# Kernel optimization log

Measured on AMD Instinct MI355X. Metric: run time of the kernel, lower is better.

Reference implementation:

```python
import jax, jax.numpy as jnp
import numpy as np

B, T, E = 4, 2048, 1024
H, D = 16, 64  # n_heads, head_size


def setup_inputs() -> dict:
    key = jax.random.key(0)
    ks = jax.random.split(key, 6)
    s = 0.02
    x = jax.random.normal(ks[0], (B, T, E), dtype=jnp.float32)
    Wq = jax.random.normal(ks[1], (H, E, D), dtype=jnp.float32) * s
    Wk = jax.random.normal(ks[2], (H, E, D), dtype=jnp.float32) * s
    Wv = jax.random.normal(ks[3], (H, E, D), dtype=jnp.float32) * s
    Wp = jax.random.normal(ks[4], (E, E), dtype=jnp.float32) * s
    bp = jnp.zeros((E,), dtype=jnp.float32)
    return {"x": x, "Wq": Wq, "Wk": Wk, "Wv": Wv, "Wp": Wp, "bp": bp}


def reference(x, Wq, Wk, Wv, Wp, bp):
    # Per-head bias-free Q/K/V projections (vectorized over heads)
    q = jnp.einsum('bte,hed->bhtd', x, Wq)
    k = jnp.einsum('bte,hed->bhtd', x, Wk)
    v = jnp.einsum('bte,hed->bhtd', x, Wv)
    scale = 1.0 / jnp.sqrt(jnp.asarray(D, dtype=x.dtype))
    scores = jnp.einsum('bhtd,bhsd->bhts', q, k) * scale  # [B,H,T,T]
    causal = jnp.tril(jnp.ones((T, T), dtype=bool))
    scores = jnp.where(causal, scores, jnp.asarray(-jnp.inf, dtype=scores.dtype))
    attn = jax.nn.softmax(scores, axis=-1)
    out = jnp.einsum('bhts,bhsd->bhtd', attn, v)  # [B,H,T,D]
    # concat heads: 'nh b t c -> b t (nh c)'
    out = out.transpose(0, 2, 1, 3).reshape(B, T, H * D)
    # output projection (dropout p=0.0 is identity)
    return out @ Wp.T + bp
```

## Files before the change

### kernel.cpp

```cpp
#include <hip/hip_runtime.h>

typedef unsigned short u16;
typedef __attribute__((ext_vector_type(8))) short bf16x8;
typedef __attribute__((ext_vector_type(4))) short bf16x4;
typedef __attribute__((ext_vector_type(4))) float f32x4;

__device__ __forceinline__ u16 f2bf(float f) {
  unsigned u = __float_as_uint(f);
  u += 0x7FFFu + ((u >> 16) & 1u);
  return (u16)(u >> 16);
}
__device__ __forceinline__ unsigned pack2(float a, float b) {
  return (unsigned)f2bf(a) | ((unsigned)f2bf(b) << 16);
}
#if __has_builtin(__builtin_amdgcn_cvt_pk_bf16_f32)
typedef __attribute__((ext_vector_type(2))) __bf16 bf16v2;
__device__ __forceinline__ unsigned cvt_pk(float a, float b) {
  bf16v2 v = __builtin_amdgcn_cvt_pk_bf16_f32(a, b);
  return __builtin_bit_cast(unsigned, v);
}
#else
__device__ __forceinline__ unsigned cvt_pk(float a, float b) { return pack2(a, b); }
#endif
__device__ __forceinline__ uint4 pack8(float4 a, float4 b) {
  uint4 r;
  r.x = cvt_pk(a.x, a.y); r.y = cvt_pk(a.z, a.w);
  r.z = cvt_pk(b.x, b.y); r.w = cvt_pk(b.z, b.w);
  return r;
}
__device__ __forceinline__ void gload16(const void* g, void* l) {
  __builtin_amdgcn_global_load_lds(
      (const __attribute__((address_space(1))) void*)g,
      (__attribute__((address_space(3))) void*)l, 16, 0, 0);
}
__device__ __forceinline__ f32x4 mfma16(bf16x4 a, bf16x4 b, f32x4 c) {
#if __has_builtin(__builtin_amdgcn_mfma_f32_16x16x16bf16_1k)
  return __builtin_amdgcn_mfma_f32_16x16x16bf16_1k(a, b, c, 0, 0, 0);
#elif __has_builtin(__builtin_amdgcn_mfma_f32_16x16x16_bf16)
  return __builtin_amdgcn_mfma_f32_16x16x16_bf16(a, b, c, 0, 0, 0);
#else
  asm volatile("v_mfma_f32_16x16x16_bf16 %0, %1, %2, %0\n\ts_nop 2"
               : "+v"(c) : "v"(a), "v"(b));
  return c;
#endif
}

__global__ __launch_bounds__(256) void prep(
    const float* __restrict__ x, u16* __restrict__ xbf,
    const float* __restrict__ Wq, const float* __restrict__ Wk,
    const float* __restrict__ Wv, u16* __restrict__ wt,
    const float* __restrict__ Wp, u16* __restrict__ wpbf) {
  const int tid = threadIdx.x;
  const int b = blockIdx.x;
  __shared__ __align__(16) u16 tile[64 * 72];
  if (b < 4096) {
    const size_t i = (size_t)b * 256 + tid;
    const float4* p = (const float4*)(x + i * 8);
    *(uint4*)(xbf + i * 8) = pack8(p[0], p[1]);
  } else if (b < 4864) {
    const int idx = b - 4096;
    const int w = idx >> 8;
    const int mat = (idx >> 4) & 15;
    const int r0 = (idx & 15) * 64;
    const float* src = (w == 0 ? Wq : (w == 1 ? Wk : Wv)) + (size_t)mat * 1024 * 64;
    u16* dst = wt + (size_t)w * 1024 * 1024 + (size_t)mat * 1024 * 64;
#pragma unroll
    for (int i = 0; i < 2; ++i) {
      const int c = tid + i * 256;
      const int r = c >> 3, off = (c & 7) * 8;
      const float* p = src + (size_t)(r0 + r) * 64 + off;
      *(uint4*)(&tile[r * 72 + off]) = pack8(*(const float4*)p, *(const float4*)(p + 4));
    }
    __syncthreads();
#pragma unroll
    for (int i = 0; i < 2; ++i) {
      const int c = tid + i * 256;
      const int d = c >> 3, roff = (c & 7) * 8;
      bf16x8 v;
#pragma unroll
      for (int j = 0; j < 8; ++j) v[j] = (short)tile[(roff + j) * 72 + d];
      *(bf16x8*)(dst + (size_t)d * 1024 + r0 + roff) = v;
    }
  } else {
    const size_t i = (size_t)(b - 4864) * 256 + tid;
    const float4* p = (const float4*)(Wp + i * 8);
    *(uint4*)(wpbf + i * 8) = pack8(p[0], p[1]);
  }
}

template <int MODE>
__global__ __launch_bounds__(256) void gemm_bt(
    const u16* __restrict__ A, const u16* __restrict__ BT,
    u16* __restrict__ o0, u16* __restrict__ o1, u16* __restrict__ o2,
    float* __restrict__ fout, const float* __restrict__ bp) {
  __shared__ __align__(16) u16 As[2][128 * 32];
  __shared__ __align__(16) u16 Bs[2][128 * 32];
  const int tid = threadIdx.x;
  const int lane = tid & 63, wv = tid >> 6;
  const int g = lane >> 4, ln = lane & 15;
  const int wm = wv >> 1, wn = wv & 1;
  const int m0 = blockIdx.x * 128, n0 = blockIdx.y * 128;

  const f32x4 fz = {0.f, 0.f, 0.f, 0.f};
  f32x4 acc[4][4];
#pragma unroll
  for (int i = 0; i < 4; ++i)
#pragma unroll
    for (int j = 0; j < 4; ++j) acc[i][j] = fz;

  for (int k0 = 0; k0 < 1024; k0 += 64) {
    __syncthreads();
#pragma unroll
    for (int hf = 0; hf < 2; ++hf)
#pragma unroll
      for (int j = 0; j < 2; ++j) {
        const int c = j * 256 + tid;
        const int r = c >> 2, off = (c & 3) * 8;
        gload16(A + (size_t)(m0 + r) * 1024 + k0 + hf * 32 + off, &As[hf][c * 8]);
        gload16(BT + (size_t)(n0 + r) * 1024 + k0 + hf * 32 + off, &Bs[hf][c * 8]);
      }
    __syncthreads();
#pragma unroll
    for (int hf = 0; hf < 2; ++hf) {
      bf16x8 af[4], bfr[4];
#pragma unroll
      for (int rt = 0; rt < 4; ++rt)
        af[rt] = *(const bf16x8*)(&As[hf][(wm * 64 + rt * 16 + ln) * 32 + g * 8]);
#pragma unroll
      for (int ct = 0; ct < 4; ++ct)
        bfr[ct] = *(const bf16x8*)(&Bs[hf][(wn * 64 + ct * 16 + ln) * 32 + g * 8]);
#pragma unroll
      for (int rt = 0; rt < 4; ++rt)
#pragma unroll
        for (int ct = 0; ct < 4; ++ct)
          acc[rt][ct] = __builtin_amdgcn_mfma_f32_16x16x32_bf16(af[rt], bfr[ct],
                                                                acc[rt][ct], 0, 0, 0);
    }
  }

  if (MODE == 0) {
    const int which = n0 >> 10;
    const int nl0 = (n0 & 1023) + wn * 64;
    const float qs = (which == 0) ? 0.1803368801f : 1.0f;
    if (which < 2) {
      u16* outp = which == 0 ? o0 : o1;
#pragma unroll
      for (int rt = 0; rt < 4; ++rt)
#pragma unroll
        for (int ct = 0; ct < 4; ++ct) {
          const int nl = nl0 + ct * 16 + ln;
          const int h = nl >> 6, d = nl & 63;
          const unsigned p01 = cvt_pk(acc[rt][ct][0] * qs, acc[rt][ct][1] * qs);
          const unsigned p23 = cvt_pk(acc[rt][ct][2] * qs, acc[rt][ct][3] * qs);
          const u16 vv[4] = {(u16)p01, (u16)(p01 >> 16), (u16)p23, (u16)(p23 >> 16)};
#pragma unroll
          for (int r = 0; r < 4; ++r) {
            const int m = m0 + wm * 64 + rt * 16 + 4 * g + r;
            const int b = m >> 11, t = m & 2047;
            outp[(((size_t)(b * 16 + h) * 2048 + t) << 6) + d] = vv[r];
          }
        }
    } else {
#pragma unroll
      for (int rt = 0; rt < 4; ++rt) {
        const int tb = m0 + wm * 64 + rt * 16 + 4 * g;
        const int b = tb >> 11, t = tb & 2047;
#pragma unroll
        for (int ct = 0; ct < 4; ++ct) {
          const int nl = nl0 + ct * 16 + ln;
          const int h = nl >> 6, d = nl & 63;
          uint2 pv;
          pv.x = cvt_pk(acc[rt][ct][0], acc[rt][ct][1]);
          pv.y = cvt_pk(acc[rt][ct][2], acc[rt][ct][3]);
          *(uint2*)(o2 + ((size_t)((b * 16 + h) * 64 + d) << 11) + t) = pv;
        }
      }
    }
  } else {
#pragma unroll
    for (int ct = 0; ct < 4; ++ct) {
      const int n = n0 + wn * 64 + ct * 16 + ln;
      const float bias = bp[n];
#pragma unroll
      for (int rt = 0; rt < 4; ++rt)
#pragma unroll
        for (int r = 0; r < 4; ++r) {
          const int m = m0 + wm * 64 + rt * 16 + 4 * g + r;
          fout[(size_t)m * 1024 + n] = acc[rt][ct][r] + bias;
        }
    }
  }
}

__global__ __launch_bounds__(256) void attn_kernel(
    const u16* __restrict__ Q, const u16* __restrict__ K,
    const u16* __restrict__ VT, u16* __restrict__ AO) {
  const int tid = threadIdx.x;
  const int wv = tid >> 6, lane = tid & 63, g = lane >> 4, ln = lane & 15;
  const int bh = blockIdx.x;
  const int jb = blockIdx.y;
  const u16* Qb = Q + (size_t)bh * (2048 * 64);
  const u16* Kb = K + (size_t)bh * (2048 * 64);
  const u16* Vb = VT + (size_t)bh * (64 * 2048);

  __shared__ __align__(16) u16 Ks[64 * 72];
  __shared__ __align__(16) u16 Vs[64 * 72];

  const int sr0 = tid >> 3, so0 = (tid & 7) * 8;
  const int sr1 = sr0 + 32;

  uint4 kpf0 = *(const uint4*)(Kb + (size_t)sr0 * 64 + so0);
  uint4 kpf1 = *(const uint4*)(Kb + (size_t)sr1 * 64 + so0);
  uint4 vpf0 = *(const uint4*)(Vb + (size_t)sr0 * 2048 + so0);
  uint4 vpf1 = *(const uint4*)(Vb + (size_t)sr1 * 2048 + so0);

  const int b = bh >> 4, h = bh & 15;
  const short ob = 0x3F80;
  const bf16x4 ones = {ob, ob, ob, ob};
  const f32x4 fz = {0.f, 0.f, 0.f, 0.f};

#pragma unroll
  for (int ph = 0; ph < 2; ++ph) {
    const int qi = (ph == 0) ? jb : 15 - jb;
    const int q0 = qi * 128;
    const int nt = 2 * qi + 2;
    const int ntw = 2 * qi + 1 + (wv >> 1);

    bf16x8 qa[2][2];
#pragma unroll
    for (int rt = 0; rt < 2; ++rt) {
      const int row = q0 + wv * 32 + rt * 16 + ln;
#pragma unroll
      for (int hh = 0; hh < 2; ++hh)
        qa[rt][hh] = *(const bf16x8*)(Qb + (size_t)row * 64 + hh * 32 + g * 8);
    }

    f32x4 oacc[2][4], lacc[2];
#pragma unroll
    for (int rt = 0; rt < 2; ++rt) {
      lacc[rt] = fz;
#pragma unroll
      for (int dt = 0; dt < 4; ++dt) oacc[rt][dt] = fz;
    }

    for (int kt = 0; kt < nt; ++kt) {
      __syncthreads();
      *(uint4*)(&Ks[sr0 * 72 + so0]) = kpf0;
      *(uint4*)(&Ks[sr1 * 72 + so0]) = kpf1;
      *(uint4*)(&Vs[sr0 * 72 + so0]) = vpf0;
      *(uint4*)(&Vs[sr1 * 72 + so0]) = vpf1;
      __syncthreads();
      if ((kt + 1 < nt) || (ph == 0)) {
        const int sn = (kt + 1 < nt) ? (kt + 1) * 64 : 0;
        kpf0 = *(const uint4*)(Kb + (size_t)(sn + sr0) * 64 + so0);
        kpf1 = *(const uint4*)(Kb + (size_t)(sn + sr1) * 64 + so0);
        vpf0 = *(const uint4*)(Vb + (size_t)sr0 * 2048 + sn + so0);
        vpf1 = *(const uint4*)(Vb + (size_t)sr1 * 2048 + sn + so0);
      }
      if (kt < ntw) {
        const int s0 = kt * 64;
        f32x4 sfT[2][4];
#pragma unroll
        for (int st = 0; st < 4; ++st) {
          const bf16x8 kb0 = *(const bf16x8*)(&Ks[(st * 16 + ln) * 72 + g * 8]);
          const bf16x8 kb1 = *(const bf16x8*)(&Ks[(st * 16 + ln) * 72 + 32 + g * 8]);
#pragma unroll
          for (int rt = 0; rt < 2; ++rt) {
            sfT[rt][st] = __builtin_amdgcn_mfma_f32_16x16x32_bf16(kb0, qa[rt][0],
                                                                  fz, 0, 0, 0);
            sfT[rt][st] = __builtin_amdgcn_mfma_f32_16x16x32_bf16(kb1, qa[rt][1],
                                                                  sfT[rt][st], 0, 0, 0);
          }
        }
        const bool diag = (kt == ntw - 1);
        bf16x4 pa[2][4];
#pragma unroll
        for (int rt = 0; rt < 2; ++rt) {
          const int qloc = wv * 32 + rt * 16 + ln;
#pragma unroll
          for (int st = 0; st < 4; ++st) {
            float e[4];
#pragma unroll
            for (int r = 0; r < 4; ++r) e[r] = __builtin_amdgcn_exp2f(sfT[rt][st][r]);
            if (diag) {
              const int sloc = s0 - q0 + st * 16 + 4 * g;
#pragma unroll
              for (int r = 0; r < 4; ++r)
                if (sloc + r > qloc) e[r] = 0.f;
            }
            uint2 packed = {cvt_pk(e[0], e[1]), cvt_pk(e[2], e[3])};
            pa[rt][st] = __builtin_bit_cast(bf16x4, packed);
          }
        }
#pragma unroll
        for (int st = 0; st < 4; ++st) {
#pragma unroll
          for (int dt = 0; dt < 4; ++dt) {
            const bf16x4 vb =
                *(const bf16x4*)(&Vs[(dt * 16 + ln) * 72 + st * 16 + 4 * g]);
#pragma unroll
            for (int rt = 0; rt < 2; ++rt)
              oacc[rt][dt] = mfma16(pa[rt][st], vb, oacc[rt][dt]);
          }
#pragma unroll
          for (int rt = 0; rt < 2; ++rt)
            lacc[rt] = mfma16(pa[rt][st], ones, lacc[rt]);
        }
      }
    }
#pragma unroll
    for (int rt = 0; rt < 2; ++rt) {
      float linv[4];
#pragma unroll
      for (int r = 0; r < 4; ++r) linv[r] = 1.f / lacc[rt][r];
#pragma unroll
      for (int dt = 0; dt < 4; ++dt) {
        const unsigned p01 =
            cvt_pk(oacc[rt][dt][0] * linv[0], oacc[rt][dt][1] * linv[1]);
        const unsigned p23 =
            cvt_pk(oacc[rt][dt][2] * linv[2], oacc[rt][dt][3] * linv[3]);
        const u16 vv[4] = {(u16)p01, (u16)(p01 >> 16), (u16)p23, (u16)(p23 >> 16)};
#pragma unroll
        for (int r = 0; r < 4; ++r) {
          const int qg = q0 + wv * 32 + rt * 16 + 4 * g + r;
          AO[(size_t)(b * 2048 + qg) * 1024 + h * 64 + dt * 16 + ln] = vv[r];
        }
      }
    }
  }
}

extern "C" void kernel_launch(void* const* d_in, const int* in_sizes, int n_in,
                              void* d_out, int out_size, void* d_ws, size_t ws_size,
                              hipStream_t stream) {
  const float* x  = (const float*)d_in[0];
  const float* Wq = (const float*)d_in[1];
  const float* Wk = (const float*)d_in[2];
  const float* Wv = (const float*)d_in[3];
  const float* Wp = (const float*)d_in[4];
  const float* bp = (const float*)d_in[5];
  float* out = (float*)d_out;

  char* ws = (char*)d_ws;
  const size_t MB = 1048576;
  u16* xbf  = (u16*)(ws);
  u16* aows = (u16*)(ws);
  u16* wt   = (u16*)(ws + 16 * MB);
  u16* wpbf = (u16*)(ws + 22 * MB);
  u16* qws  = (u16*)(ws + 24 * MB);
  u16* kws  = (u16*)(ws + 40 * MB);
  u16* vtws = (u16*)(ws + 56 * MB);

  prep<<<dim3(5376), 256, 0, stream>>>(x, xbf, Wq, Wk, Wv, wt, Wp, wpbf);
  gemm_bt<0><<<dim3(64, 24), 256, 0, stream>>>(xbf, wt, qws, kws, vtws,
                                               nullptr, nullptr);
  attn_kernel<<<dim3(64, 8), 256, 0, stream>>>(qws, kws, vtws, aows);
  gemm_bt<1><<<dim3(64, 8), 256, 0, stream>>>(aows, wpbf, nullptr, nullptr,
                                              nullptr, out, bp);
}
```

Before: 263.4 us.

## Process both paired query blocks in one pass sharing K/V tile loads

The attention kernel previously ran two sequential phases, one for the light query block and one for the mirrored heavy block, reloading K/V tiles from global memory for each. It now keeps Q fragments and accumulators for both blocks live and streams K/V once over the longer range, applying QK, exp/mask and PV for each block only where it is still active. This removes the duplicate K/V global loads and LDS staging, and halves the barrier count for the shorter block. In exchange, register pressure roughly doubles for accumulators and Q fragments, which can lower occupancy or cause spills.

```diff
diff --git a/kernel.cpp b/kernel.cpp
--- a/kernel.cpp
+++ b/kernel.cpp
@@ -209,105 +209,134 @@
   const int sr0 = tid >> 3, so0 = (tid & 7) * 8;
   const int sr1 = sr0 + 32;
 
+  const int qiA = jb, qiB = 15 - jb;
+  const int q0A = qiA * 128, q0B = qiB * 128;
+  const int ntB = 2 * qiB + 2;
+  const int ntwA = 2 * qiA + 1 + (wv >> 1);
+  const int ntwB = 2 * qiB + 1 + (wv >> 1);
+
   uint4 kpf0 = *(const uint4*)(Kb + (size_t)sr0 * 64 + so0);
   uint4 kpf1 = *(const uint4*)(Kb + (size_t)sr1 * 64 + so0);
   uint4 vpf0 = *(const uint4*)(Vb + (size_t)sr0 * 2048 + so0);
   uint4 vpf1 = *(const uint4*)(Vb + (size_t)sr1 * 2048 + so0);
 
-  const int b = bh >> 4, h = bh & 15;
+  bf16x8 qaA[2][2], qaB[2][2];
+#pragma unroll
+  for (int rt = 0; rt < 2; ++rt) {
+    const int rowA = q0A + wv * 32 + rt * 16 + ln;
+    const int rowB = q0B + wv * 32 + rt * 16 + ln;
+#pragma unroll
+    for (int hh = 0; hh < 2; ++hh) {
+      qaA[rt][hh] = *(const bf16x8*)(Qb + (size_t)rowA * 64 + hh * 32 + g * 8);
+      qaB[rt][hh] = *(const bf16x8*)(Qb + (size_t)rowB * 64 + hh * 32 + g * 8);
+    }
+  }
+
+  const f32x4 fz = {0.f, 0.f, 0.f, 0.f};
+  f32x4 oaccA[2][4], oaccB[2][4], laccA[2], laccB[2];
+#pragma unroll
+  for (int rt = 0; rt < 2; ++rt) {
+    laccA[rt] = fz; laccB[rt] = fz;
+#pragma unroll
+    for (int dt = 0; dt < 4; ++dt) { oaccA[rt][dt] = fz; oaccB[rt][dt] = fz; }
+  }
+
   const short ob = 0x3F80;
   const bf16x4 ones = {ob, ob, ob, ob};
-  const f32x4 fz = {0.f, 0.f, 0.f, 0.f};
-
-#pragma unroll
-  for (int ph = 0; ph < 2; ++ph) {
-    const int qi = (ph == 0) ? jb : 15 - jb;
-    const int q0 = qi * 128;
-    const int nt = 2 * qi + 2;
-    const int ntw = 2 * qi + 1 + (wv >> 1);
-
-    bf16x8 qa[2][2];
+
+  auto expmask = [&](f32x4 (&sf)[2][4], bf16x4 (&pa)[2][4], bool diag, int s0q) {
 #pragma unroll
     for (int rt = 0; rt < 2; ++rt) {
-      const int row = q0 + wv * 32 + rt * 16 + ln;
-#pragma unroll
-      for (int hh = 0; hh < 2; ++hh)
-        qa[rt][hh] = *(const bf16x8*)(Qb + (size_t)row * 64 + hh * 32 + g * 8);
-    }
-
-    f32x4 oacc[2][4], lacc[2];
-#pragma unroll
-    for (int rt = 0; rt < 2; ++rt) {
-      lacc[rt] = fz;
-#pragma unroll
-      for (int dt = 0; dt < 4; ++dt) oacc[rt][dt] = fz;
-    }
-
-    for (int kt = 0; kt < nt; ++kt) {
-      __syncthreads();
-      *(uint4*)(&Ks[sr0 * 72 + so0]) = kpf0;
-      *(uint4*)(&Ks[sr1 * 72 + so0]) = kpf1;
-      *(uint4*)(&Vs[sr0 * 72 + so0]) = vpf0;
-      *(uint4*)(&Vs[sr1 * 72 + so0]) = vpf1;
-      __syncthreads();
-      if ((kt + 1 < nt) || (ph == 0)) {
-        const int sn = (kt + 1 < nt) ? (kt + 1) * 64 : 0;
-        kpf0 = *(const uint4*)(Kb + (size_t)(sn + sr0) * 64 + so0);
-        kpf1 = *(const uint4*)(Kb + (size_t)(sn + sr1) * 64 + so0);
-        vpf0 = *(const uint4*)(Vb + (size_t)sr0 * 2048 + sn + so0);
-        vpf1 = *(const uint4*)(Vb + (size_t)sr1 * 2048 + sn + so0);
-      }
-      if (kt < ntw) {
-        const int s0 = kt * 64;
-        f32x4 sfT[2][4];
-#pragma unroll
-        for (int st = 0; st < 4; ++st) {
-          const bf16x8 kb0 = *(const bf16x8*)(&Ks[(st * 16 + ln) * 72 + g * 8]);
-          const bf16x8 kb1 = *(const bf16x8*)(&Ks[(st * 16 + ln) * 72 + 32 + g * 8]);
-#pragma unroll
-          for (int rt = 0; rt < 2; ++rt) {
-            sfT[rt][st] = __builtin_amdgcn_mfma_f32_16x16x32_bf16(kb0, qa[rt][0],
-                                                                  fz, 0, 0, 0);
-            sfT[rt][st] = __builtin_amdgcn_mfma_f32_16x16x32_bf16(kb1, qa[rt][1],
-                                                                  sfT[rt][st], 0, 0, 0);
-          }
-        }
-        const bool diag = (kt == ntw - 1);
-        bf16x4 pa[2][4];
+      const int qloc = wv * 32 + rt * 16 + ln;
+#pragma unroll
+      for (int st = 0; st < 4; ++st) {
+        float e[4];
+#pragma unroll
+        for (int r = 0; r < 4; ++r) e[r] = __builtin_amdgcn_exp2f(sf[rt][st][r]);
+        if (diag) {
+          const int sloc = s0q + st * 16 + 4 * g;
+#pragma unroll
+          for (int r = 0; r < 4; ++r)
+            if (sloc + r > qloc) e[r] = 0.f;
+        }
+        uint2 packed = {cvt_pk(e[0], e[1]), cvt_pk(e[2], e[3])};
+        pa[rt][st] = __builtin_bit_cast(bf16x4, packed);
+      }
+    }
+  };
+
+  for (int kt = 0; kt < ntB; ++kt) {
+    __syncthreads();
+    *(uint4*)(&Ks[sr0 * 72 + so0]) = kpf0;
+    *(uint4*)(&Ks[sr1 * 72 + so0]) = kpf1;
+    *(uint4*)(&Vs[sr0 * 72 + so0]) = vpf0;
+    *(uint4*)(&Vs[sr1 * 72 + so0]) = vpf1;
+    __syncthreads();
+    if (kt + 1 < ntB) {
+      const int sn = (kt + 1) * 64;
+      kpf0 = *(const uint4*)(Kb + (size_t)(sn + sr0) * 64 + so0);
+      kpf1 = *(const uint4*)(Kb + (size_t)(sn + sr1) * 64 + so0);
+      vpf0 = *(const uint4*)(Vb + (size_t)sr0 * 2048 + sn + so0);
+      vpf1 = *(const uint4*)(Vb + (size_t)sr1 * 2048 + sn + so0);
+    }
+    const bool actA = kt < ntwA;
+    const bool actB = kt < ntwB;
+
+    f32x4 sfA[2][4], sfB[2][4];
+#pragma unroll
+    for (int st = 0; st < 4; ++st) {
+      const bf16x8 kb0 = *(const bf16x8*)(&Ks[(st * 16 + ln) * 72 + g * 8]);
+      const bf16x8 kb1 = *(const bf16x8*)(&Ks[(st * 16 + ln) * 72 + 32 + g * 8]);
+      if (actA)
 #pragma unroll
         for (int rt = 0; rt < 2; ++rt) {
-          const int qloc = wv * 32 + rt * 16 + ln;
-#pragma unroll
-          for (int st = 0; st < 4; ++st) {
-            float e[4];
-#pragma unroll
-            for (int r = 0; r < 4; ++r) e[r] = __builtin_amdgcn_exp2f(sfT[rt][st][r]);
-            if (diag) {
-              const int sloc = s0 - q0 + st * 16 + 4 * g;
-#pragma unroll
-              for (int r = 0; r < 4; ++r)
-                if (sloc + r > qloc) e[r] = 0.f;
-            }
-            uint2 packed = {cvt_pk(e[0], e[1]), cvt_pk(e[2], e[3])};
-            pa[rt][st] = __builtin_bit_cast(bf16x4, packed);
-          }
-        }
-#pragma unroll
-        for (int st = 0; st < 4; ++st) {
-#pragma unroll
-          for (int dt = 0; dt < 4; ++dt) {
-            const bf16x4 vb =
-                *(const bf16x4*)(&Vs[(dt * 16 + ln) * 72 + st * 16 + 4 * g]);
-#pragma unroll
-            for (int rt = 0; rt < 2; ++rt)
-              oacc[rt][dt] = mfma16(pa[rt][st], vb, oacc[rt][dt]);
-          }
+          sfA[rt][st] = __builtin_amdgcn_mfma_f32_16x16x32_bf16(kb0, qaA[rt][0],
+                                                                fz, 0, 0, 0);
+          sfA[rt][st] = __builtin_amdgcn_mfma_f32_16x16x32_bf16(kb1, qaA[rt][1],
+                                                                sfA[rt][st], 0, 0, 0);
+        }
+      if (actB)
+#pragma unroll
+        for (int rt = 0; rt < 2; ++rt) {
+          sfB[rt][st] = __builtin_amdgcn_mfma_f32_16x16x32_bf16(kb0, qaB[rt][0],
+                                                                fz, 0, 0, 0);
+          sfB[rt][st] = __builtin_amdgcn_mfma_f32_16x16x32_bf16(kb1, qaB[rt][1],
+                                                                sfB[rt][st], 0, 0, 0);
+        }
+    }
+    bf16x4 paA[2][4], paB[2][4];
+    const int s0 = kt * 64;
+    if (actA) expmask(sfA, paA, kt == ntwA - 1, s0 - q0A);
+    if (actB) expmask(sfB, paB, kt == ntwB - 1, s0 - q0B);
+
+#pragma unroll
+    for (int st = 0; st < 4; ++st) {
+#pragma unroll
+      for (int dt = 0; dt < 4; ++dt) {
+        const bf16x4 vb =
+            *(const bf16x4*)(&Vs[(dt * 16 + ln) * 72 + st * 16 + 4 * g]);
+        if (actA)
 #pragma unroll
           for (int rt = 0; rt < 2; ++rt)
-            lacc[rt] = mfma16(pa[rt][st], ones, lacc[rt]);
-        }
-      }
-    }
+            oaccA[rt][dt] = mfma16(paA[rt][st], vb, oaccA[rt][dt]);
+        if (actB)
+#pragma unroll
+          for (int rt = 0; rt < 2; ++rt)
+            oaccB[rt][dt] = mfma16(paB[rt][st], vb, oaccB[rt][dt]);
+      }
+      if (actA)
+#pragma unroll
+        for (int rt = 0; rt < 2; ++rt)
+          laccA[rt] = mfma16(paA[rt][st], ones, laccA[rt]);
+      if (actB)
+#pragma unroll
+        for (int rt = 0; rt < 2; ++rt)
+          laccB[rt] = mfma16(paB[rt][st], ones, laccB[rt]);
+    }
+  }
+
+  const int b = bh >> 4, h = bh & 15;
+  auto epi = [&](f32x4 (&oacc)[2][4], f32x4 (&lacc)[2], int q0) {
 #pragma unroll
     for (int rt = 0; rt < 2; ++rt) {
       float linv[4];
@@ -327,7 +356,9 @@
         }
       }
     }
-  }
+  };
+  epi(oaccA, laccA, q0A);
+  epi(oaccB, laccB, q0B);
 }
 
 extern "C" void kernel_launch(void* const* d_in, const int* in_sizes, int n_in,
```

Measured after the change: 320.9 us. +21.8%, slower.

## Load K/V fragments directly from global memory instead of staging through LDS

Applied to the files above, without the earlier changes.

The attention kernel drops the shared-memory K/V tiles, the register prefetch and both block barriers per key tile. Each wave now reads its K and V^T MFMA fragments straight from global memory and loops only over its own key-tile count, so waves no longer synchronise. The point is to remove barrier stalls and LDS traffic. In exchange, each wave issues redundant global loads (four waves read the same K/V data and rely on L1/L2 hits), and there is no software prefetch to hide load latency.

```diff
diff --git a/kernel.cpp b/kernel.cpp
--- a/kernel.cpp
+++ b/kernel.cpp
@@ -203,27 +203,18 @@
   const u16* Kb = K + (size_t)bh * (2048 * 64);
   const u16* Vb = VT + (size_t)bh * (64 * 2048);
 
-  __shared__ __align__(16) u16 Ks[64 * 72];
-  __shared__ __align__(16) u16 Vs[64 * 72];
-
-  const int sr0 = tid >> 3, so0 = (tid & 7) * 8;
-  const int sr1 = sr0 + 32;
-
-  uint4 kpf0 = *(const uint4*)(Kb + (size_t)sr0 * 64 + so0);
-  uint4 kpf1 = *(const uint4*)(Kb + (size_t)sr1 * 64 + so0);
-  uint4 vpf0 = *(const uint4*)(Vb + (size_t)sr0 * 2048 + so0);
-  uint4 vpf1 = *(const uint4*)(Vb + (size_t)sr1 * 2048 + so0);
-
   const int b = bh >> 4, h = bh & 15;
   const short ob = 0x3F80;
   const bf16x4 ones = {ob, ob, ob, ob};
   const f32x4 fz = {0.f, 0.f, 0.f, 0.f};
 
+  const u16* kp0 = Kb + (size_t)ln * 64 + g * 8;
+  const u16* vp0 = Vb + (size_t)ln * 2048 + 4 * g;
+
 #pragma unroll
   for (int ph = 0; ph < 2; ++ph) {
     const int qi = (ph == 0) ? jb : 15 - jb;
     const int q0 = qi * 128;
-    const int nt = 2 * qi + 2;
     const int ntw = 2 * qi + 1 + (wv >> 1);
 
     bf16x8 qa[2][2];
@@ -243,69 +234,55 @@
       for (int dt = 0; dt < 4; ++dt) oacc[rt][dt] = fz;
     }
 
-    for (int kt = 0; kt < nt; ++kt) {
-      __syncthreads();
-      *(uint4*)(&Ks[sr0 * 72 + so0]) = kpf0;
-      *(uint4*)(&Ks[sr1 * 72 + so0]) = kpf1;
-      *(uint4*)(&Vs[sr0 * 72 + so0]) = vpf0;
-      *(uint4*)(&Vs[sr1 * 72 + so0]) = vpf1;
-      __syncthreads();
-      if ((kt + 1 < nt) || (ph == 0)) {
-        const int sn = (kt + 1 < nt) ? (kt + 1) * 64 : 0;
-        kpf0 = *(const uint4*)(Kb + (size_t)(sn + sr0) * 64 + so0);
-        kpf1 = *(const uint4*)(Kb + (size_t)(sn + sr1) * 64 + so0);
-        vpf0 = *(const uint4*)(Vb + (size_t)sr0 * 2048 + sn + so0);
-        vpf1 = *(const uint4*)(Vb + (size_t)sr1 * 2048 + sn + so0);
-      }
-      if (kt < ntw) {
-        const int s0 = kt * 64;
-        f32x4 sfT[2][4];
+    for (int kt = 0; kt < ntw; ++kt) {
+      const int s0 = kt * 64;
+      f32x4 sfT[2][4];
+#pragma unroll
+      for (int st = 0; st < 4; ++st) {
+        const u16* kr = kp0 + (size_t)(s0 + st * 16) * 64;
+        const bf16x8 kb0 = *(const bf16x8*)(kr);
+        const bf16x8 kb1 = *(const bf16x8*)(kr + 32);
+#pragma unroll
+        for (int rt = 0; rt < 2; ++rt) {
+          sfT[rt][st] = __builtin_amdgcn_mfma_f32_16x16x32_bf16(kb0, qa[rt][0],
+                                                                fz, 0, 0, 0);
+          sfT[rt][st] = __builtin_amdgcn_mfma_f32_16x16x32_bf16(kb1, qa[rt][1],
+                                                                sfT[rt][st], 0, 0, 0);
+        }
+      }
+      const bool diag = (kt == ntw - 1);
+      bf16x4 pa[2][4];
+#pragma unroll
+      for (int rt = 0; rt < 2; ++rt) {
+        const int qloc = wv * 32 + rt * 16 + ln;
 #pragma unroll
         for (int st = 0; st < 4; ++st) {
-          const bf16x8 kb0 = *(const bf16x8*)(&Ks[(st * 16 + ln) * 72 + g * 8]);
-          const bf16x8 kb1 = *(const bf16x8*)(&Ks[(st * 16 + ln) * 72 + 32 + g * 8]);
-#pragma unroll
-          for (int rt = 0; rt < 2; ++rt) {
-            sfT[rt][st] = __builtin_amdgcn_mfma_f32_16x16x32_bf16(kb0, qa[rt][0],
-                                                                  fz, 0, 0, 0);
-            sfT[rt][st] = __builtin_amdgcn_mfma_f32_16x16x32_bf16(kb1, qa[rt][1],
-                                                                  sfT[rt][st], 0, 0, 0);
+          float e[4];
+#pragma unroll
+          for (int r = 0; r < 4; ++r) e[r] = __builtin_amdgcn_exp2f(sfT[rt][st][r]);
+          if (diag) {
+            const int sloc = s0 - q0 + st * 16 + 4 * g;
+#pragma unroll
+            for (int r = 0; r < 4; ++r)
+              if (sloc + r > qloc) e[r] = 0.f;
           }
-        }
-        const bool diag = (kt == ntw - 1);
-        bf16x4 pa[2][4];
-#pragma unroll
-        for (int rt = 0; rt < 2; ++rt) {
-          const int qloc = wv * 32 + rt * 16 + ln;
-#pragma unroll
-          for (int st = 0; st < 4; ++st) {
-            float e[4];
-#pragma unroll
-            for (int r = 0; r < 4; ++r) e[r] = __builtin_amdgcn_exp2f(sfT[rt][st][r]);
-            if (diag) {
-              const int sloc = s0 - q0 + st * 16 + 4 * g;
-#pragma unroll
-              for (int r = 0; r < 4; ++r)
-                if (sloc + r > qloc) e[r] = 0.f;
-            }
-            uint2 packed = {cvt_pk(e[0], e[1]), cvt_pk(e[2], e[3])};
-            pa[rt][st] = __builtin_bit_cast(bf16x4, packed);
-          }
-        }
-#pragma unroll
-        for (int st = 0; st < 4; ++st) {
-#pragma unroll
-          for (int dt = 0; dt < 4; ++dt) {
-            const bf16x4 vb =
-                *(const bf16x4*)(&Vs[(dt * 16 + ln) * 72 + st * 16 + 4 * g]);
-#pragma unroll
-            for (int rt = 0; rt < 2; ++rt)
-              oacc[rt][dt] = mfma16(pa[rt][st], vb, oacc[rt][dt]);
-          }
+          uint2 packed = {cvt_pk(e[0], e[1]), cvt_pk(e[2], e[3])};
+          pa[rt][st] = __builtin_bit_cast(bf16x4, packed);
+        }
+      }
+#pragma unroll
+      for (int st = 0; st < 4; ++st) {
+#pragma unroll
+        for (int dt = 0; dt < 4; ++dt) {
+          const bf16x4 vb =
+              *(const bf16x4*)(vp0 + (size_t)dt * 16 * 2048 + s0 + st * 16);
 #pragma unroll
           for (int rt = 0; rt < 2; ++rt)
-            lacc[rt] = mfma16(pa[rt][st], ones, lacc[rt]);
-        }
+            oacc[rt][dt] = mfma16(pa[rt][st], vb, oacc[rt][dt]);
+        }
+#pragma unroll
+        for (int rt = 0; rt < 2; ++rt)
+          lacc[rt] = mfma16(pa[rt][st], ones, lacc[rt]);
       }
     }
 #pragma unroll
```

After: 381.0 us. 44.7% more time.
